# Performance work log

Hardware: AMD Instinct MI355X
Metric: run time of the kernel (lower is better)

Reference implementation:

```python
import jax, jax.numpy as jnp
import numpy as np

B, N, F, I = 4, 1024, 32, 8
DIM, DN, NF = 256, 64, 100
H, HD = 4, 64  # heads, head_dim (H*HD == DIM)
EPS = 1e-5


def setup_inputs() -> dict:
    key = jax.random.key(0)
    ks = jax.random.split(key, 24)
    def p(k, shape, s=0.05):
        return jax.random.normal(k, shape, jnp.float32) * s
    return {
        "x": jax.random.normal(ks[0], (B, N, F, I), jnp.float32),
        "idx": jax.random.randint(ks[1], (F,), 0, NF),
        "ctx": jax.random.normal(ks[2], (B, 1, DN), jnp.float32),
        "Wp": p(ks[3], (NF, DIM * I)),          # in_projection table
        "Bp": p(ks[4], (NF, DIM)),               # feature_bias table
        "q_emb": p(ks[5], (1, DIM)),             # queries table
        "cln_kv_W": p(ks[6], (DN, 2 * DIM)), "cln_kv_b": jnp.zeros((2 * DIM,), jnp.float32),
        "cln_q_W": p(ks[7], (DN, 2 * DIM)),  "cln_q_b": jnp.zeros((2 * DIM,), jnp.float32),
        "cln_h_W": p(ks[8], (DN, 2 * DIM)),  "cln_h_b": jnp.zeros((2 * DIM,), jnp.float32),
        "Wq": p(ks[9], (DIM, DIM)), "Wk": p(ks[10], (DIM, DIM)),
        "Wv": p(ks[11], (DIM, DIM)), "Wo": p(ks[12], (DIM, DIM)),
        "W1": p(ks[13], (DIM, 4 * DIM)), "b1": jnp.zeros((4 * DIM,), jnp.float32),
        "W2": p(ks[14], (4 * DIM, DIM)), "b2": jnp.zeros((DIM,), jnp.float32),
    }


def _ln(x):
    m = x.mean(-1, keepdims=True)
    v = ((x - m) ** 2).mean(-1, keepdims=True)
    return (x - m) * jax.lax.rsqrt(v + EPS)


def _cln(x, c, W, b):
    # adaptive layernorm: ln(x) * (1 + scale(ctx)) + shift(ctx)
    h = _ln(x)
    s, sh = jnp.split(c @ W + b, 2, axis=-1)
    return h * (1.0 + s) + sh


def reference(x, idx, ctx, Wp, Bp, q_emb, cln_kv_W, cln_kv_b, cln_q_W, cln_q_b,
              cln_h_W, cln_h_b, Wq, Wk, Wv, Wo, W1, b1, W2, b2):
    b_, n_, f_, i_ = x.shape
    # gather per-feature projection weights and biases
    w = Wp[idx].reshape(f_, DIM, i_)                 # [f, d, i]
    bias = Bp[idx][None]                              # [1, f, d] (broadcasts b,n)
    kv = jnp.einsum('bnfi,fdi->bnfd', x, w)           # [b, n, f, d]
    c = ctx[:, :, None, :]                            # [b, 1, 1, dn]
    kv = _cln(kv, c, cln_kv_W, cln_kv_b) + bias
    q = jnp.broadcast_to(q_emb[None, None], (b_, n_, 1, DIM))
    # cross-attention (pre-norm, conditional)
    qn = _cln(q, c, cln_q_W, cln_q_b)
    qh = (qn @ Wq).reshape(b_, n_, 1, H, HD)
    kh = (kv @ Wk).reshape(b_, n_, f_, H, HD)
    vh = (kv @ Wv).reshape(b_, n_, f_, H, HD)
    att = jnp.einsum('bnqhe,bnfhe->bnhqf', qh, kh) / np.sqrt(HD).astype(np.float32)
    att = jax.nn.softmax(att, axis=-1)
    o = jnp.einsum('bnhqf,bnfhe->bnqhe', att, vh).reshape(b_, n_, 1, DIM) @ Wo
    h = q + o
    # MLP (pre-norm, conditional)
    hn = _cln(h, c, cln_h_W, cln_h_b)
    h = h + (jax.nn.gelu(hn @ W1 + b1) @ W2 + b2)
    return h[:, :, 0, :]                              # squeeze query dim -> [b, n, d]
```

## Files before the change

### kernel.cpp

```cpp
#include <hip/hip_runtime.h>
#include <cmath>

#define EPSV 1e-5f
using f4 = float4;

typedef __attribute__((ext_vector_type(8))) short bfrag;
typedef __attribute__((ext_vector_type(4))) float ffrag;

#define WS_SKV   0
#define WS_SHKV  1024
#define WS_SH    2048
#define WS_SHH   3072
#define WS_A     4096
#define WS_R     8192
#define WS_HT    4202496
#define WS_L     5251072
#define WS_G     6299648
#define WS_GB    WS_G
#define WS_HNB   (WS_G + 2097152)
#define WS_W1T   (WS_G + 2621440)
#define WS_W2T   (WS_G + 2752512)
#define WS_MT    (WS_G + 2883584)

#define FMA8(acc, s, wa, wb) \
  acc[0]=fmaf((s),(wa).x,acc[0]); acc[1]=fmaf((s),(wa).y,acc[1]); \
  acc[2]=fmaf((s),(wa).z,acc[2]); acc[3]=fmaf((s),(wa).w,acc[3]); \
  acc[4]=fmaf((s),(wb).x,acc[4]); acc[5]=fmaf((s),(wb).y,acc[5]); \
  acc[6]=fmaf((s),(wb).z,acc[6]); acc[7]=fmaf((s),(wb).w,acc[7]);

#define DOT8(res, v, wa, wb) \
  res = fmaf((v)[0],(wa).x,res); res = fmaf((v)[1],(wa).y,res); \
  res = fmaf((v)[2],(wa).z,res); res = fmaf((v)[3],(wa).w,res); \
  res = fmaf((v)[4],(wb).x,res); res = fmaf((v)[5],(wb).y,res); \
  res = fmaf((v)[6],(wb).z,res); res = fmaf((v)[7],(wb).w,res);

__device__ __forceinline__ float bfly32(float v){
  v += __shfl_xor(v, 1);  v += __shfl_xor(v, 2);  v += __shfl_xor(v, 4);
  v += __shfl_xor(v, 8);  v += __shfl_xor(v, 16);
  return v;
}

template<int CTRL>
__device__ __forceinline__ float dpp_add(float v){
  int x = __builtin_bit_cast(int, v);
  int y = __builtin_amdgcn_update_dpp(0, x, CTRL, 0xf, 0xf, true);
  return v + __builtin_bit_cast(float, y);
}
__device__ __forceinline__ float red32(float v){
  v = dpp_add<0xB1>(v);
  v = dpp_add<0x4E>(v);
  v = dpp_add<0x124>(v);
  v = dpp_add<0x128>(v);
  v += __shfl_xor(v, 16);
  return v;
}

__device__ __forceinline__ float gelu_fast(float x){
  float z2 = 1.5957691216057308f*(x + 0.044715f*x*x*x);
  return x / (1.0f + __expf(-z2));
}

__device__ __forceinline__ unsigned short f2bf(float x){
  union { float f; unsigned u; } v; v.f = x;
  unsigned r = v.u + 0x7fffu + ((v.u >> 16) & 1u);
  return (unsigned short)(r >> 16);
}
__device__ __forceinline__ float bfu(unsigned short u){
  union { unsigned u; float f; } v; v.u = ((unsigned)u) << 16; return v.f;
}
__device__ __forceinline__ ushort4 comb4(ushort4 a, ushort4 b, float inv){
  ushort4 r;
  r.x = f2bf((bfu(a.x)+bfu(b.x))*inv);
  r.y = f2bf((bfu(a.y)+bfu(b.y))*inv);
  r.z = f2bf((bfu(a.z)+bfu(b.z))*inv);
  r.w = f2bf((bfu(a.w)+bfu(b.w))*inv);
  return r;
}

__global__ __launch_bounds__(256) void kwm_conv(
  const float* __restrict__ W1, const float* __restrict__ W2,
  const float* __restrict__ Wv, const float* __restrict__ Wo,
  float* __restrict__ ws)
{
  const int tid = threadIdx.x;
  int blk = blockIdx.x;
  if (blk < 128){
    __shared__ unsigned short lt[64][68];
    const float* src; unsigned short* dst; int K, N, K0, N0;
    if (blk < 64){
      src = W1; dst = (unsigned short*)(ws + WS_W1T);
      K = 256; N = 1024; K0 = (blk >> 4)*64; N0 = (blk & 15)*64;
    } else {
      blk -= 64;
      src = W2; dst = (unsigned short*)(ws + WS_W2T);
      K = 1024; N = 256; K0 = (blk >> 2)*64; N0 = (blk & 3)*64;
    }
    #pragma unroll
    for (int i=0;i<4;++i){
      int r = i*16 + (tid>>4);
      int c = (tid&15)*4;
      f4 v = *(const f4*)(src + (size_t)(K0+r)*N + N0 + c);
      lt[r][c]   = f2bf(v.x); lt[r][c+1] = f2bf(v.y);
      lt[r][c+2] = f2bf(v.z); lt[r][c+3] = f2bf(v.w);
    }
    __syncthreads();
    #pragma unroll
    for (int i=0;i<4;++i){
      int n  = i*16 + (tid>>4);
      int kc = (tid&15)*4;
      ushort4 u;
      u.x = lt[kc][n]; u.y = lt[kc+1][n]; u.z = lt[kc+2][n]; u.w = lt[kc+3][n];
      *(ushort4*)(dst + (size_t)(N0+n)*K + K0 + kc) = u;
    }
  } else {
    blk -= 128;
    __shared__ float wvs[4*64];
    __shared__ float wos[64*256];
    const int h   = blk >> 6;
    const int dg4 = blk & 63;
    {
      int d = tid >> 6, e = tid & 63;
      wvs[d*64+e] = Wv[(size_t)(dg4*4 + d)*256 + h*64 + e];
    }
    {
      int e = tid >> 2, c = (tid & 3)*64;
      const float* src = Wo + (size_t)(h*64 + e)*256 + c;
      #pragma unroll
      for (int i=0;i<16;++i)
        *(f4*)&wos[e*256 + c + i*4] = *(const f4*)(src + i*4);
    }
    __syncthreads();
    float acc[4] = {};
    for (int e=0;e<64;++e){
      float wo = wos[e*256 + tid];
      acc[0] = fmaf(wvs[0*64+e], wo, acc[0]);
      acc[1] = fmaf(wvs[1*64+e], wo, acc[1]);
      acc[2] = fmaf(wvs[2*64+e], wo, acc[2]);
      acc[3] = fmaf(wvs[3*64+e], wo, acc[3]);
    }
    unsigned short* Mt = (unsigned short*)(ws + WS_MT);
    ushort4 u;
    u.x = f2bf(acc[0]); u.y = f2bf(acc[1]); u.z = f2bf(acc[2]); u.w = f2bf(acc[3]);
    *(ushort4*)(Mt + (size_t)tid*1024 + h*256 + dg4*4) = u;
  }
}

__global__ __launch_bounds__(256) void k0_all(
    const float* __restrict__ ctx, const float* __restrict__ q_emb,
    const float* __restrict__ Wkv, const float* __restrict__ bkv,
    const float* __restrict__ Wqc, const float* __restrict__ bqc,
    const float* __restrict__ Whc, const float* __restrict__ bhc,
    const float* __restrict__ Wq,  const float* __restrict__ Wk,
    float* __restrict__ ws)
{
  const int b = blockIdx.x >> 2, h = blockIdx.x & 3;
  const int tid = threadIdx.x;
  __shared__ float c[64], qn[256], ph[256], qh64[64], red[8];
  if (tid < 64) c[tid] = ctx[b*64 + tid];
  __syncthreads();

  float skv = bkv[tid],      shkv = bkv[256+tid];
  float sq  = bqc[tid],      shq  = bqc[256+tid];
  float sh  = bhc[tid],      shh  = bhc[256+tid];
  #pragma unroll 8
  for (int j=0;j<64;++j){
    float cj = c[j];
    skv  = fmaf(cj, Wkv[j*512 + tid],       skv);
    shkv = fmaf(cj, Wkv[j*512 + 256 + tid], shkv);
    sq   = fmaf(cj, Wqc[j*512 + tid],       sq);
    shq  = fmaf(cj, Wqc[j*512 + 256 + tid], shq);
    sh   = fmaf(cj, Whc[j*512 + tid],       sh);
    shh  = fmaf(cj, Whc[j*512 + 256 + tid], shh);
  }
  if (h == 0){
    ws[WS_SKV  + b*256 + tid] = skv;
    ws[WS_SHKV + b*256 + tid] = shkv;
    ws[WS_SH   + b*256 + tid] = sh;
    ws[WS_SHH  + b*256 + tid] = shh;
  }

  float qe = q_emb[tid];
  float s1r = qe, s2r = qe*qe;
  for (int mm=1;mm<64;mm<<=1){ s1r += __shfl_xor(s1r,mm); s2r += __shfl_xor(s2r,mm); }
  int wv = tid>>6, ln = tid&63;
  if (ln==0){ red[wv*2]=s1r; red[wv*2+1]=s2r; }
  __syncthreads();
  float S1 = red[0]+red[2]+red[4]+red[6];
  float S2 = red[1]+red[3]+red[5]+red[7];
  float mean = S1*(1.0f/256.0f);
  float var  = S2*(1.0f/256.0f) - mean*mean;
  float rs   = rsqrtf(var + EPSV);
  qn[tid] = (qe-mean)*rs*(1.0f+sq) + shq;
  __syncthreads();

  {
    const int t = tid & 63, ks = tid >> 6;
    float p = 0.f;
    const float* wq = Wq + (size_t)(ks*64)*256 + h*64 + t;
    #pragma unroll 8
    for (int d=0; d<64; ++d) p = fmaf(qn[ks*64+d], wq[d*256], p);
    ph[tid] = p;
  }
  __syncthreads();
  if (tid < 64) qh64[tid] = ph[tid] + ph[64+tid] + ph[128+tid] + ph[192+tid];
  __syncthreads();

  {
    float a = 0.f;
    const float* wkr = Wk + (size_t)tid*256 + h*64;
    #pragma unroll
    for (int e4=0; e4<16; ++e4){
      f4 wv4 = *(const f4*)(wkr + e4*4);
      a = fmaf(qh64[e4*4+0], wv4.x, a);
      a = fmaf(qh64[e4*4+1], wv4.y, a);
      a = fmaf(qh64[e4*4+2], wv4.z, a);
      a = fmaf(qh64[e4*4+3], wv4.w, a);
    }
    ws[WS_A + b*1024 + h*256 + tid] = 0.125f*a;
  }
}

__global__ __launch_bounds__(256,4) void k1f_attn(
  const float* __restrict__ x, const int* __restrict__ idx,
  const float* __restrict__ Wp, const float* __restrict__ Bp,
  float* __restrict__ ws)
{
  __shared__ float xs[2048];
  __shared__ float wls[4096];

  const int tid = threadIdx.x;
  const int p0  = (blockIdx.x >> 1) * 8;
  const int half= blockIdx.x & 1;
  const int f0  = half * 16;
  const int b   = p0 >> 10;
  const int t   = tid >> 5;
  const int dg  = tid & 31;
  const int dA  = 4*dg, dB = 128 + 4*dg;

  {
    const float* xg = x + (size_t)p0*256 + tid*8;
    f4 a  = *(const f4*)xg;
    f4 bq = *(const f4*)(xg + 4);
    *(f4*)&xs[tid*8]     = a;
    *(f4*)&xs[tid*8 + 4] = bq;
  }
  f4 Ar[4][2];
  #pragma unroll
  for (int h=0;h<4;++h){
    Ar[h][0] = *(const f4*)(ws + WS_A + b*1024 + h*256 + dA);
    Ar[h][1] = *(const f4*)(ws + WS_A + b*1024 + h*256 + dB);
  }

  f4 skA = *(const f4*)(ws + WS_SKV  + b*256 + dA);
  f4 skB = *(const f4*)(ws + WS_SKV  + b*256 + dB);
  f4 shA = *(const f4*)(ws + WS_SHKV + b*256 + dA);
  f4 shB = *(const f4*)(ws + WS_SHKV + b*256 + dB);
  float coef[8] = {1.f+skA.x,1.f+skA.y,1.f+skA.z,1.f+skA.w,
                   1.f+skB.x,1.f+skB.y,1.f+skB.z,1.f+skB.w};
  float shk[8]  = {shA.x,shA.y,shA.z,shA.w, shB.x,shB.y,shB.z,shB.w};

  int r0 = idx[f0], r1 = idx[f0+1];
  f4 u0 = *(const f4*)(Wp + (size_t)r0*2048 + tid*8);
  f4 u1 = *(const f4*)(Wp + (size_t)r0*2048 + tid*8 + 4);
  f4 u2 = *(const f4*)(Wp + (size_t)r1*2048 + tid*8);
  f4 u3 = *(const f4*)(Wp + (size_t)r1*2048 + tid*8 + 4);

  float l[4] = {0.f,0.f,0.f,0.f};
  float racc[4][8] = {};

  for (int fi = 0; fi < 8; ++fi){
    const int f = f0 + fi*2;
    __syncthreads();
    wls[0*256+tid]=u0.x; wls[1*256+tid]=u0.y; wls[2*256+tid]=u0.z; wls[3*256+tid]=u0.w;
    wls[4*256+tid]=u1.x; wls[5*256+tid]=u1.y; wls[6*256+tid]=u1.z; wls[7*256+tid]=u1.w;
    wls[2048+0*256+tid]=u2.x; wls[2048+1*256+tid]=u2.y;
    wls[2048+2*256+tid]=u2.z; wls[2048+3*256+tid]=u2.w;
    wls[2048+4*256+tid]=u3.x; wls[2048+5*256+tid]=u3.y;
    wls[2048+6*256+tid]=u3.z; wls[2048+7*256+tid]=u3.w;
    __syncthreads();

    f4 ba0 = *(const f4*)(Bp + (size_t)r0*256 + dA);
    f4 bb0 = *(const f4*)(Bp + (size_t)r0*256 + dB);
    f4 ba1 = *(const f4*)(Bp + (size_t)r1*256 + dA);
    f4 bb1 = *(const f4*)(Bp + (size_t)r1*256 + dB);

    const int fn = (fi < 7) ? f + 2 : f0;
    int rn0 = idx[fn], rn1 = idx[fn+1];
    u0 = *(const f4*)(Wp + (size_t)rn0*2048 + tid*8);
    u1 = *(const f4*)(Wp + (size_t)rn0*2048 + tid*8 + 4);
    u2 = *(const f4*)(Wp + (size_t)rn1*2048 + tid*8);
    u3 = *(const f4*)(Wp + (size_t)rn1*2048 + tid*8 + 4);

    #pragma unroll
    for (int sub=0; sub<2; ++sub){
      const float* wrow = wls + sub*2048;
      const int fc = f + sub;
      f4 ba = sub ? ba1 : ba0;
      f4 bb = sub ? bb1 : bb0;

      f4 xa = *(const f4*)&xs[t*256 + fc*8];
      f4 xb = *(const f4*)&xs[t*256 + fc*8 + 4];
      float xf[8] = {xa.x,xa.y,xa.z,xa.w, xb.x,xb.y,xb.z,xb.w};

      float val[8] = {};
      #pragma unroll
      for (int i=0;i<8;++i){
        f4 wa  = *(const f4*)&wrow[i*256 + dA];
        f4 wbv = *(const f4*)&wrow[i*256 + dB];
        FMA8(val, xf[i], wa, wbv);
      }

      float s=0.f, ss=0.f;
      #pragma unroll
      for (int jj=0;jj<8;++jj){ s += val[jj]; ss = fmaf(val[jj],val[jj],ss); }
      s = red32(s); ss = red32(ss);
      float mean = s*(1.f/256.f);
      float var  = ss*(1.f/256.f) - mean*mean;
      float rsg  = rsqrtf(var + EPSV);
      float mrs  = mean*rsg;

      float off[8] = {shk[0]+ba.x, shk[1]+ba.y, shk[2]+ba.z, shk[3]+ba.w,
                      shk[4]+bb.x, shk[5]+bb.y, shk[6]+bb.z, shk[7]+bb.w};
      float kvl[8];
      #pragma unroll
      for (int jj=0;jj<8;++jj)
        kvl[jj] = fmaf(fmaf(val[jj], rsg, -mrs), coef[jj], off[jj]);

      #pragma unroll
      for (int h=0;h<4;++h){
        float lg = 0.f;
        DOT8(lg, kvl, Ar[h][0], Ar[h][1]);
        lg = red32(lg);
        float pp = __expf(lg);
        l[h] += pp;
        #pragma unroll
        for (int jj=0;jj<8;++jj)
          racc[h][jj] = fmaf(pp, kvl[jj], racc[h][jj]);
      }
    }
    r0 = rn0; r1 = rn1;
  }

  unsigned short* Pr = (unsigned short*)(ws + WS_R);
  size_t base = (size_t)(half*4096 + p0 + t) * 1024;
  #pragma unroll
  for (int h=0;h<4;++h){
    ushort4 ua, ub;
    ua.x=f2bf(racc[h][0]); ua.y=f2bf(racc[h][1]); ua.z=f2bf(racc[h][2]); ua.w=f2bf(racc[h][3]);
    ub.x=f2bf(racc[h][4]); ub.y=f2bf(racc[h][5]); ub.z=f2bf(racc[h][6]); ub.w=f2bf(racc[h][7]);
    *(ushort4*)(Pr + base + h*256 + dA) = ua;
    *(ushort4*)(Pr + base + h*256 + dB) = ub;
  }
  if (dg == 0){
    float* Lp = ws + WS_L;
    #pragma unroll
    for (int h=0;h<4;++h) Lp[(size_t)(half*4096 + p0 + t)*4 + h] = l[h];
  }
}

__global__ __launch_bounds__(256) void k2g_mfma(float* __restrict__ ws)
{
  __shared__ unsigned short aT[2][32*40];
  __shared__ unsigned short bT[2][64*40];
  __shared__ float invs[128];
  const unsigned short* P0 = (const unsigned short*)(ws + WS_R);
  const unsigned short* P1 = P0 + 4194304;
  const unsigned short* mt = (const unsigned short*)(ws + WS_MT);
  const float* Lp = ws + WS_L;

  const int tid = threadIdx.x;
  const int M0 = (blockIdx.x >> 2) * 32;
  const int N0 = (blockIdx.x & 3) * 64;
  const int lane = tid & 63;
  const int wid = tid >> 6;
  const int wm = wid >> 1, wn = wid & 1;
  const int m16 = lane & 15, q = lane >> 4;

  const int sa_m = tid >> 3, sa_k = (tid & 7) * 4;
  const int sb_n = tid >> 2, sb_k = (tid & 3) * 8;

  if (tid < 128){
    int lt = tid >> 2, h = tid & 3;
    invs[tid] = 1.f / (Lp[(size_t)(M0 + lt)*4 + h] +
                       Lp[(size_t)(4096 + M0 + lt)*4 + h]);
  }

  ushort4 ua0 = *(const ushort4*)(P0 + (size_t)(M0 + sa_m)*1024 + sa_k);
  ushort4 ua1 = *(const ushort4*)(P1 + (size_t)(M0 + sa_m)*1024 + sa_k);
  f4 ub = *(const f4*)(mt + (size_t)(N0 + sb_n)*1024 + sb_k);
  __syncthreads();

  ffrag acc[2];
  acc[0] = (ffrag){0.f,0.f,0.f,0.f};
  acc[1] = (ffrag){0.f,0.f,0.f,0.f};

  for (int ks=0; ks<32; ++ks){
    const int buf = ks & 1;
    float inv = invs[sa_m*4 + (ks >> 3)];
    *(ushort4*)&aT[buf][sa_m*40 + sa_k] = comb4(ua0, ua1, inv);
    *(f4*)&bT[buf][sb_n*40 + sb_k]      = ub;
    __syncthreads();
    int kn = (ks < 31) ? ks+1 : 31;
    ua0 = *(const ushort4*)(P0 + (size_t)(M0 + sa_m)*1024 + kn*32 + sa_k);
    ua1 = *(const ushort4*)(P1 + (size_t)(M0 + sa_m)*1024 + kn*32 + sa_k);
    ub  = *(const f4*)(mt + (size_t)(N0 + sb_n)*1024 + kn*32 + sb_k);

    bfrag af, bf0, bf1;
    af  = *(const bfrag*)&aT[buf][(wm*16 + m16)*40 + q*8];
    bf0 = *(const bfrag*)&bT[buf][(wn*32 + m16)*40 + q*8];
    bf1 = *(const bfrag*)&bT[buf][(wn*32 + 16 + m16)*40 + q*8];
    acc[0] = __builtin_amdgcn_mfma_f32_16x16x32_bf16(bf0, af, acc[0], 0, 0, 0);
    acc[1] = __builtin_amdgcn_mfma_f32_16x16x32_bf16(bf1, af, acc[1], 0, 0, 0);
  }

  const int m = M0 + wm*16 + m16;
  #pragma unroll
  for (int j=0;j<2;++j){
    const int n4 = N0 + wn*32 + j*16 + q*4;
    *(f4*)(ws + WS_HT + (size_t)m*256 + n4) =
      make_float4(acc[j][0], acc[j][1], acc[j][2], acc[j][3]);
  }
}

__global__ __launch_bounds__(256) void ke_ln(
  const float* __restrict__ q_emb, float* __restrict__ ws)
{
  const int tid = threadIdx.x;
  const int p0 = blockIdx.x * 8;
  const int b  = p0 >> 10;
  const int tq = tid >> 5, jq = tid & 31;
  const int cA = 4*jq, cB = 128 + 4*jq;

  float* op = ws + WS_HT + (size_t)(p0+tq)*256;
  f4 oA = *(const f4*)(op + cA);
  f4 oB = *(const f4*)(op + cB);
  f4 qA = *(const f4*)(q_emb + cA);
  f4 qB = *(const f4*)(q_emb + cB);
  float ht[8] = {oA.x+qA.x, oA.y+qA.y, oA.z+qA.z, oA.w+qA.w,
                 oB.x+qB.x, oB.y+qB.y, oB.z+qB.z, oB.w+qB.w};
  float s=0.f, ss=0.f;
  #pragma unroll
  for (int jj=0;jj<8;++jj){ s += ht[jj]; ss = fmaf(ht[jj],ht[jj],ss); }
  s = bfly32(s); ss = bfly32(ss);
  float mean = s*(1.f/256.f);
  float var  = ss*(1.f/256.f) - mean*mean;
  float rsg  = rsqrtf(var + EPSV);
  f4 sH0 = *(const f4*)(ws + WS_SH  + b*256 + cA);
  f4 sH1 = *(const f4*)(ws + WS_SH  + b*256 + cB);
  f4 hH0 = *(const f4*)(ws + WS_SHH + b*256 + cA);
  f4 hH1 = *(const f4*)(ws + WS_SHH + b*256 + cB);
  float sHv[8]  = {sH0.x,sH0.y,sH0.z,sH0.w, sH1.x,sH1.y,sH1.z,sH1.w};
  float hHv[8]  = {hH0.x,hH0.y,hH0.z,hH0.w, hH1.x,hH1.y,hH1.z,hH1.w};
  float hnv[8];
  #pragma unroll
  for (int jj=0;jj<8;++jj)
    hnv[jj] = (ht[jj]-mean)*rsg*(1.f+sHv[jj]) + hHv[jj];

  *(f4*)(op+cA) = make_float4(ht[0],ht[1],ht[2],ht[3]);
  *(f4*)(op+cB) = make_float4(ht[4],ht[5],ht[6],ht[7]);
  unsigned short* hnb = (unsigned short*)(ws + WS_HNB);
  ushort4 uA, uB;
  uA.x=f2bf(hnv[0]); uA.y=f2bf(hnv[1]); uA.z=f2bf(hnv[2]); uA.w=f2bf(hnv[3]);
  uB.x=f2bf(hnv[4]); uB.y=f2bf(hnv[5]); uB.z=f2bf(hnv[6]); uB.w=f2bf(hnv[7]);
  *(ushort4*)(hnb + (size_t)(p0+tq)*256 + cA) = uA;
  *(ushort4*)(hnb + (size_t)(p0+tq)*256 + cB) = uB;
}

__global__ __launch_bounds__(256) void k3_mfma(
  const float* __restrict__ b1, float* __restrict__ ws)
{
  __shared__ unsigned short aT[2][64*40];
  __shared__ unsigned short bT[2][128*40];
  const unsigned short* hnb = (const unsigned short*)(ws + WS_HNB);
  const unsigned short* w1t = (const unsigned short*)(ws + WS_W1T);
  unsigned short* gb = (unsigned short*)(ws + WS_GB);

  const int tid = threadIdx.x;
  const int M0 = (blockIdx.x >> 3) * 64;
  const int N0 = (blockIdx.x & 7) * 128;
  const int lane = tid & 63;
  const int wid = tid >> 6;
  const int wm = wid >> 1, wn = wid & 1;
  const int m16 = lane & 15, q = lane >> 4;

  const int sa_m = tid >> 2, sa_k = (tid & 3) * 8;
  const int sb_n = tid >> 1, sb_k = (tid & 1) * 16;

  f4 ua, ub0, ub1;
  ua  = *(const f4*)(hnb + (size_t)(M0 + sa_m)*256 + sa_k);
  ub0 = *(const f4*)(w1t + (size_t)(N0 + sb_n)*256 + sb_k);
  ub1 = *(const f4*)(w1t + (size_t)(N0 + sb_n)*256 + sb_k + 8);

  ffrag acc[2][4];
  #pragma unroll
  for (int i=0;i<2;++i)
    #pragma unroll
    for (int j=0;j<4;++j) acc[i][j] = (ffrag){0.f,0.f,0.f,0.f};

  for (int ks=0; ks<8; ++ks){
    const int buf = ks & 1;
    *(f4*)&aT[buf][sa_m*40 + sa_k]     = ua;
    *(f4*)&bT[buf][sb_n*40 + sb_k]     = ub0;
    *(f4*)&bT[buf][sb_n*40 + sb_k + 8] = ub1;
    __syncthreads();
    int kn = (ks < 7) ? ks+1 : 7;
    ua  = *(const f4*)(hnb + (size_t)(M0 + sa_m)*256 + kn*32 + sa_k);
    ub0 = *(const f4*)(w1t + (size_t)(N0 + sb_n)*256 + kn*32 + sb_k);
    ub1 = *(const f4*)(w1t + (size_t)(N0 + sb_n)*256 + kn*32 + sb_k + 8);

    bfrag af[2], bf_[4];
    af[0] = *(const bfrag*)&aT[buf][(wm*32 + m16)*40 + q*8];
    af[1] = *(const bfrag*)&aT[buf][(wm*32 + 16 + m16)*40 + q*8];
    #pragma unroll
    for (int j=0;j<4;++j)
      bf_[j] = *(const bfrag*)&bT[buf][(wn*64 + j*16 + m16)*40 + q*8];
    #pragma unroll
    for (int i=0;i<2;++i)
      #pragma unroll
      for (int j=0;j<4;++j)
        acc[i][j] = __builtin_amdgcn_mfma_f32_16x16x32_bf16(bf_[j], af[i], acc[i][j], 0, 0, 0);
  }

  #pragma unroll
  for (int i=0;i<2;++i){
    const int m = M0 + wm*32 + i*16 + m16;
    #pragma unroll
    for (int j=0;j<4;++j){
      const int n4 = N0 + wn*64 + j*16 + q*4;
      f4 bv = *(const f4*)(b1 + n4);
      ushort4 u;
      u.x = f2bf(gelu_fast(acc[i][j][0] + bv.x));
      u.y = f2bf(gelu_fast(acc[i][j][1] + bv.y));
      u.z = f2bf(gelu_fast(acc[i][j][2] + bv.z));
      u.w = f2bf(gelu_fast(acc[i][j][3] + bv.w));
      *(ushort4*)(gb + (size_t)m*1024 + n4) = u;
    }
  }
}

__global__ __launch_bounds__(256) void k4_mfma(
  const float* __restrict__ b2, const float* __restrict__ ws_c,
  float* __restrict__ ws, float* __restrict__ out)
{
  __shared__ unsigned short aT[2][32*40];
  __shared__ unsigned short bT[2][64*40];
  const unsigned short* gb  = (const unsigned short*)(ws_c + WS_GB);
  const unsigned short* w2t = (const unsigned short*)(ws_c + WS_W2T);

  const int tid = threadIdx.x;
  const int M0 = (blockIdx.x >> 2) * 32;
  const int N0 = (blockIdx.x & 3) * 64;
  const int lane = tid & 63;
  const int wid = tid >> 6;
  const int wm = wid >> 1, wn = wid & 1;
  const int m16 = lane & 15, q = lane >> 4;

  const int sa_m = tid >> 3, sa_k = (tid & 7) * 4;
  const int sb_n = tid >> 2, sb_k = (tid & 3) * 8;

  ushort4 ua;
  f4 ub;
  ua = *(const ushort4*)(gb  + (size_t)(M0 + sa_m)*1024 + sa_k);
  ub = *(const f4*)(w2t + (size_t)(N0 + sb_n)*1024 + sb_k);

  ffrag acc[2];
  acc[0] = (ffrag){0.f,0.f,0.f,0.f};
  acc[1] = (ffrag){0.f,0.f,0.f,0.f};

  for (int ks=0; ks<32; ++ks){
    const int buf = ks & 1;
    *(ushort4*)&aT[buf][sa_m*40 + sa_k] = ua;
    *(f4*)&bT[buf][sb_n*40 + sb_k]      = ub;
    __syncthreads();
    int kn = (ks < 31) ? ks+1 : 31;
    ua = *(const ushort4*)(gb  + (size_t)(M0 + sa_m)*1024 + kn*32 + sa_k);
    ub = *(const f4*)(w2t + (size_t)(N0 + sb_n)*1024 + kn*32 + sb_k);

    bfrag af, bf0, bf1;
    af  = *(const bfrag*)&aT[buf][(wm*16 + m16)*40 + q*8];
    bf0 = *(const bfrag*)&bT[buf][(wn*32 + m16)*40 + q*8];
    bf1 = *(const bfrag*)&bT[buf][(wn*32 + 16 + m16)*40 + q*8];
    acc[0] = __builtin_amdgcn_mfma_f32_16x16x32_bf16(bf0, af, acc[0], 0, 0, 0);
    acc[1] = __builtin_amdgcn_mfma_f32_16x16x32_bf16(bf1, af, acc[1], 0, 0, 0);
  }

  const int m = M0 + wm*16 + m16;
  #pragma unroll
  for (int j=0;j<2;++j){
    const int n4 = N0 + wn*32 + j*16 + q*4;
    f4 bv = *(const f4*)(b2 + n4);
    f4 hv = *(const f4*)(ws + WS_HT + (size_t)m*256 + n4);
    *(f4*)(out + (size_t)m*256 + n4) =
      make_float4(acc[j][0]+bv.x+hv.x, acc[j][1]+bv.y+hv.y,
                  acc[j][2]+bv.z+hv.z, acc[j][3]+bv.w+hv.w);
  }
}

extern "C" void kernel_launch(void* const* d_in, const int* in_sizes, int n_in,
                              void* d_out, int out_size, void* d_ws, size_t ws_size,
                              hipStream_t stream)
{
  const float* x    = (const float*)d_in[0];
  const int*   idx  = (const int*)  d_in[1];
  const float* ctx  = (const float*)d_in[2];
  const float* Wp   = (const float*)d_in[3];
  const float* Bp   = (const float*)d_in[4];
  const float* qemb = (const float*)d_in[5];
  const float* Wkv  = (const float*)d_in[6];
  const float* bkv  = (const float*)d_in[7];
  const float* Wqc  = (const float*)d_in[8];
  const float* bqc  = (const float*)d_in[9];
  const float* Whc  = (const float*)d_in[10];
  const float* bhc  = (const float*)d_in[11];
  const float* Wq   = (const float*)d_in[12];
  const float* Wk   = (const float*)d_in[13];
  const float* Wv   = (const float*)d_in[14];
  const float* Wo   = (const float*)d_in[15];
  const float* W1   = (const float*)d_in[16];
  const float* b1   = (const float*)d_in[17];
  const float* W2   = (const float*)d_in[18];
  const float* b2   = (const float*)d_in[19];
  float* ws  = (float*)d_ws;
  float* out = (float*)d_out;

  hipLaunchKernelGGL(kwm_conv, dim3(384),  dim3(256), 0, stream, W1, W2, Wv, Wo, ws);
  hipLaunchKernelGGL(k0_all,   dim3(16),   dim3(256), 0, stream,
                     ctx, qemb, Wkv, bkv, Wqc, bqc, Whc, bhc, Wq, Wk, ws);
  hipLaunchKernelGGL(k1f_attn, dim3(1024), dim3(256), 0, stream, x, idx, Wp, Bp, ws);
  hipLaunchKernelGGL(k2g_mfma, dim3(512),  dim3(256), 0, stream, ws);
  hipLaunchKernelGGL(ke_ln,    dim3(512),  dim3(256), 0, stream, qemb, ws);
  hipLaunchKernelGGL(k3_mfma,  dim3(512),  dim3(256), 0, stream, b1, ws);
  hipLaunchKernelGGL(k4_mfma,  dim3(512),  dim3(256), 0, stream, b2, ws, ws, out);
}
```

Baseline: 193.8 us.

## Merge prep kernels and process two token rows per thread in attention kernel

Folds the context/query precompute kernel into the weight-conversion kernel as extra blocks sharing a union of shared memory, removing one launch. The attention kernel now handles 16 tokens per block (two per thread) so each weight row read from shared memory is reused for two tokens, halving the grid. This raises register pressure (launch bounds lowered to 2 blocks per SM) and cuts parallelism to 512 blocks, which may hurt latency hiding.

Measured after the change: 187.0 us. 3.5% less time.

```diff
diff --git a/kernel.cpp b/kernel.cpp
--- a/kernel.cpp
+++ b/kernel.cpp
@@ -77,15 +77,25 @@
   return r;
 }
 
-__global__ __launch_bounds__(256) void kwm_conv(
+__global__ __launch_bounds__(256) void kprep(
   const float* __restrict__ W1, const float* __restrict__ W2,
   const float* __restrict__ Wv, const float* __restrict__ Wo,
+  const float* __restrict__ ctx, const float* __restrict__ q_emb,
+  const float* __restrict__ Wkv, const float* __restrict__ bkv,
+  const float* __restrict__ Wqc, const float* __restrict__ bqc,
+  const float* __restrict__ Whc, const float* __restrict__ bhc,
+  const float* __restrict__ Wq,  const float* __restrict__ Wk,
   float* __restrict__ ws)
 {
   const int tid = threadIdx.x;
   int blk = blockIdx.x;
+  __shared__ union {
+    unsigned short lt[64][68];
+    struct { float wvs[4*64]; float wos[64*256]; } m;
+    struct { float c[64], qn[256], ph[256], qh64[64], red[8]; } z;
+  } sm;
+
   if (blk < 128){
-    __shared__ unsigned short lt[64][68];
     const float* src; unsigned short* dst; int K, N, K0, N0;
     if (blk < 64){
       src = W1; dst = (unsigned short*)(ws + WS_W1T);
@@ -100,8 +110,8 @@
       int r = i*16 + (tid>>4);
       int c = (tid&15)*4;
       f4 v = *(const f4*)(src + (size_t)(K0+r)*N + N0 + c);
-      lt[r][c]   = f2bf(v.x); lt[r][c+1] = f2bf(v.y);
-      lt[r][c+2] = f2bf(v.z); lt[r][c+3] = f2bf(v.w);
+      sm.lt[r][c]   = f2bf(v.x); sm.lt[r][c+1] = f2bf(v.y);
+      sm.lt[r][c+2] = f2bf(v.z); sm.lt[r][c+3] = f2bf(v.w);
     }
     __syncthreads();
     #pragma unroll
@@ -109,127 +119,115 @@
       int n  = i*16 + (tid>>4);
       int kc = (tid&15)*4;
       ushort4 u;
-      u.x = lt[kc][n]; u.y = lt[kc+1][n]; u.z = lt[kc+2][n]; u.w = lt[kc+3][n];
+      u.x = sm.lt[kc][n]; u.y = sm.lt[kc+1][n]; u.z = sm.lt[kc+2][n]; u.w = sm.lt[kc+3][n];
       *(ushort4*)(dst + (size_t)(N0+n)*K + K0 + kc) = u;
     }
-  } else {
+  } else if (blk < 384){
     blk -= 128;
-    __shared__ float wvs[4*64];
-    __shared__ float wos[64*256];
     const int h   = blk >> 6;
     const int dg4 = blk & 63;
     {
       int d = tid >> 6, e = tid & 63;
-      wvs[d*64+e] = Wv[(size_t)(dg4*4 + d)*256 + h*64 + e];
+      sm.m.wvs[d*64+e] = Wv[(size_t)(dg4*4 + d)*256 + h*64 + e];
     }
     {
       int e = tid >> 2, c = (tid & 3)*64;
       const float* src = Wo + (size_t)(h*64 + e)*256 + c;
       #pragma unroll
       for (int i=0;i<16;++i)
-        *(f4*)&wos[e*256 + c + i*4] = *(const f4*)(src + i*4);
+        *(f4*)&sm.m.wos[e*256 + c + i*4] = *(const f4*)(src + i*4);
     }
     __syncthreads();
     float acc[4] = {};
     for (int e=0;e<64;++e){
-      float wo = wos[e*256 + tid];
-      acc[0] = fmaf(wvs[0*64+e], wo, acc[0]);
-      acc[1] = fmaf(wvs[1*64+e], wo, acc[1]);
-      acc[2] = fmaf(wvs[2*64+e], wo, acc[2]);
-      acc[3] = fmaf(wvs[3*64+e], wo, acc[3]);
+      float wo = sm.m.wos[e*256 + tid];
+      acc[0] = fmaf(sm.m.wvs[0*64+e], wo, acc[0]);
+      acc[1] = fmaf(sm.m.wvs[1*64+e], wo, acc[1]);
+      acc[2] = fmaf(sm.m.wvs[2*64+e], wo, acc[2]);
+      acc[3] = fmaf(sm.m.wvs[3*64+e], wo, acc[3]);
     }
     unsigned short* Mt = (unsigned short*)(ws + WS_MT);
     ushort4 u;
     u.x = f2bf(acc[0]); u.y = f2bf(acc[1]); u.z = f2bf(acc[2]); u.w = f2bf(acc[3]);
     *(ushort4*)(Mt + (size_t)tid*1024 + h*256 + dg4*4) = u;
-  }
-}
-
-__global__ __launch_bounds__(256) void k0_all(
-    const float* __restrict__ ctx, const float* __restrict__ q_emb,
-    const float* __restrict__ Wkv, const float* __restrict__ bkv,
-    const float* __restrict__ Wqc, const float* __restrict__ bqc,
-    const float* __restrict__ Whc, const float* __restrict__ bhc,
-    const float* __restrict__ Wq,  const float* __restrict__ Wk,
-    float* __restrict__ ws)
-{
-  const int b = blockIdx.x >> 2, h = blockIdx.x & 3;
-  const int tid = threadIdx.x;
-  __shared__ float c[64], qn[256], ph[256], qh64[64], red[8];
-  if (tid < 64) c[tid] = ctx[b*64 + tid];
-  __syncthreads();
-
-  float skv = bkv[tid],      shkv = bkv[256+tid];
-  float sq  = bqc[tid],      shq  = bqc[256+tid];
-  float sh  = bhc[tid],      shh  = bhc[256+tid];
-  #pragma unroll 8
-  for (int j=0;j<64;++j){
-    float cj = c[j];
-    skv  = fmaf(cj, Wkv[j*512 + tid],       skv);
-    shkv = fmaf(cj, Wkv[j*512 + 256 + tid], shkv);
-    sq   = fmaf(cj, Wqc[j*512 + tid],       sq);
-    shq  = fmaf(cj, Wqc[j*512 + 256 + tid], shq);
-    sh   = fmaf(cj, Whc[j*512 + tid],       sh);
-    shh  = fmaf(cj, Whc[j*512 + 256 + tid], shh);
-  }
-  if (h == 0){
-    ws[WS_SKV  + b*256 + tid] = skv;
-    ws[WS_SHKV + b*256 + tid] = shkv;
-    ws[WS_SH   + b*256 + tid] = sh;
-    ws[WS_SHH  + b*256 + tid] = shh;
-  }
-
-  float qe = q_emb[tid];
-  float s1r = qe, s2r = qe*qe;
-  for (int mm=1;mm<64;mm<<=1){ s1r += __shfl_xor(s1r,mm); s2r += __shfl_xor(s2r,mm); }
-  int wv = tid>>6, ln = tid&63;
-  if (ln==0){ red[wv*2]=s1r; red[wv*2+1]=s2r; }
-  __syncthreads();
-  float S1 = red[0]+red[2]+red[4]+red[6];
-  float S2 = red[1]+red[3]+red[5]+red[7];
-  float mean = S1*(1.0f/256.0f);
-  float var  = S2*(1.0f/256.0f) - mean*mean;
-  float rs   = rsqrtf(var + EPSV);
-  qn[tid] = (qe-mean)*rs*(1.0f+sq) + shq;
-  __syncthreads();
-
-  {
-    const int t = tid & 63, ks = tid >> 6;
-    float p = 0.f;
-    const float* wq = Wq + (size_t)(ks*64)*256 + h*64 + t;
+  } else {
+    blk -= 384;
+    const int b = blk >> 2, h = blk & 3;
+    if (tid < 64) sm.z.c[tid] = ctx[b*64 + tid];
+    __syncthreads();
+
+    float skv = bkv[tid],      shkv = bkv[256+tid];
+    float sq  = bqc[tid],      shq  = bqc[256+tid];
+    float sh  = bhc[tid],      shh  = bhc[256+tid];
     #pragma unroll 8
-    for (int d=0; d<64; ++d) p = fmaf(qn[ks*64+d], wq[d*256], p);
-    ph[tid] = p;
-  }
-  __syncthreads();
-  if (tid < 64) qh64[tid] = ph[tid] + ph[64+tid] + ph[128+tid] + ph[192+tid];
-  __syncthreads();
-
-  {
-    float a = 0.f;
-    const float* wkr = Wk + (size_t)tid*256 + h*64;
-    #pragma unroll
-    for (int e4=0; e4<16; ++e4){
-      f4 wv4 = *(const f4*)(wkr + e4*4);
-      a = fmaf(qh64[e4*4+0], wv4.x, a);
-      a = fmaf(qh64[e4*4+1], wv4.y, a);
-      a = fmaf(qh64[e4*4+2], wv4.z, a);
-      a = fmaf(qh64[e4*4+3], wv4.w, a);
-    }
-    ws[WS_A + b*1024 + h*256 + tid] = 0.125f*a;
-  }
-}
-
-__global__ __launch_bounds__(256,4) void k1f_attn(
+    for (int j=0;j<64;++j){
+      float cj = sm.z.c[j];
+      skv  = fmaf(cj, Wkv[j*512 + tid],       skv);
+      shkv = fmaf(cj, Wkv[j*512 + 256 + tid], shkv);
+      sq   = fmaf(cj, Wqc[j*512 + tid],       sq);
+      shq  = fmaf(cj, Wqc[j*512 + 256 + tid], shq);
+      sh   = fmaf(cj, Whc[j*512 + tid],       sh);
+      shh  = fmaf(cj, Whc[j*512 + 256 + tid], shh);
+    }
+    if (h == 0){
+      ws[WS_SKV  + b*256 + tid] = skv;
+      ws[WS_SHKV + b*256 + tid] = shkv;
+      ws[WS_SH   + b*256 + tid] = sh;
+      ws[WS_SHH  + b*256 + tid] = shh;
+    }
+
+    float qe = q_emb[tid];
+    float s1r = qe, s2r = qe*qe;
+    for (int mm=1;mm<64;mm<<=1){ s1r += __shfl_xor(s1r,mm); s2r += __shfl_xor(s2r,mm); }
+    int wv = tid>>6, ln = tid&63;
+    if (ln==0){ sm.z.red[wv*2]=s1r; sm.z.red[wv*2+1]=s2r; }
+    __syncthreads();
+    float S1 = sm.z.red[0]+sm.z.red[2]+sm.z.red[4]+sm.z.red[6];
+    float S2 = sm.z.red[1]+sm.z.red[3]+sm.z.red[5]+sm.z.red[7];
+    float mean = S1*(1.0f/256.0f);
+    float var  = S2*(1.0f/256.0f) - mean*mean;
+    float rs   = rsqrtf(var + EPSV);
+    sm.z.qn[tid] = (qe-mean)*rs*(1.0f+sq) + shq;
+    __syncthreads();
+
+    {
+      const int t = tid & 63, ks = tid >> 6;
+      float p = 0.f;
+      const float* wq = Wq + (size_t)(ks*64)*256 + h*64 + t;
+      #pragma unroll 8
+      for (int d=0; d<64; ++d) p = fmaf(sm.z.qn[ks*64+d], wq[d*256], p);
+      sm.z.ph[tid] = p;
+    }
+    __syncthreads();
+    if (tid < 64) sm.z.qh64[tid] = sm.z.ph[tid] + sm.z.ph[64+tid] + sm.z.ph[128+tid] + sm.z.ph[192+tid];
+    __syncthreads();
+
+    {
+      float a = 0.f;
+      const float* wkr = Wk + (size_t)tid*256 + h*64;
+      #pragma unroll
+      for (int e4=0; e4<16; ++e4){
+        f4 wv4 = *(const f4*)(wkr + e4*4);
+        a = fmaf(sm.z.qh64[e4*4+0], wv4.x, a);
+        a = fmaf(sm.z.qh64[e4*4+1], wv4.y, a);
+        a = fmaf(sm.z.qh64[e4*4+2], wv4.z, a);
+        a = fmaf(sm.z.qh64[e4*4+3], wv4.w, a);
+      }
+      ws[WS_A + b*1024 + h*256 + tid] = 0.125f*a;
+    }
+  }
+}
+
+__global__ __launch_bounds__(256,2) void k1f_attn(
   const float* __restrict__ x, const int* __restrict__ idx,
   const float* __restrict__ Wp, const float* __restrict__ Bp,
   float* __restrict__ ws)
 {
-  __shared__ float xs[2048];
+  __shared__ float xs[4096];
   __shared__ float wls[4096];
 
   const int tid = threadIdx.x;
-  const int p0  = (blockIdx.x >> 1) * 8;
+  const int p0  = (blockIdx.x >> 1) * 16;
   const int half= blockIdx.x & 1;
   const int f0  = half * 16;
   const int b   = p0 >> 10;
@@ -243,6 +241,10 @@
     f4 bq = *(const f4*)(xg + 4);
     *(f4*)&xs[tid*8]     = a;
     *(f4*)&xs[tid*8 + 4] = bq;
+    f4 a2  = *(const f4*)(xg + 2048);
+    f4 bq2 = *(const f4*)(xg + 2048 + 4);
+    *(f4*)&xs[2048 + tid*8]     = a2;
+    *(f4*)&xs[2048 + tid*8 + 4] = bq2;
   }
   f4 Ar[4][2];
   #pragma unroll
@@ -265,8 +267,8 @@
   f4 u2 = *(const f4*)(Wp + (size_t)r1*2048 + tid*8);
   f4 u3 = *(const f4*)(Wp + (size_t)r1*2048 + tid*8 + 4);
 
-  float l[4] = {0.f,0.f,0.f,0.f};
-  float racc[4][8] = {};
+  float l[2][4] = {};
+  float racc[2][4][8] = {};
 
   for (int fi = 0; fi < 8; ++fi){
     const int f = f0 + fi*2;
@@ -298,63 +300,84 @@
       f4 ba = sub ? ba1 : ba0;
       f4 bb = sub ? bb1 : bb0;
 
-      f4 xa = *(const f4*)&xs[t*256 + fc*8];
-      f4 xb = *(const f4*)&xs[t*256 + fc*8 + 4];
-      float xf[8] = {xa.x,xa.y,xa.z,xa.w, xb.x,xb.y,xb.z,xb.w};
-
-      float val[8] = {};
+      float xf0[8], xf1[8];
+      {
+        f4 xa = *(const f4*)&xs[t*256 + fc*8];
+        f4 xb = *(const f4*)&xs[t*256 + fc*8 + 4];
+        xf0[0]=xa.x; xf0[1]=xa.y; xf0[2]=xa.z; xf0[3]=xa.w;
+        xf0[4]=xb.x; xf0[5]=xb.y; xf0[6]=xb.z; xf0[7]=xb.w;
+        f4 xc = *(const f4*)&xs[(t+8)*256 + fc*8];
+        f4 xd = *(const f4*)&xs[(t+8)*256 + fc*8 + 4];
+        xf1[0]=xc.x; xf1[1]=xc.y; xf1[2]=xc.z; xf1[3]=xc.w;
+        xf1[4]=xd.x; xf1[5]=xd.y; xf1[6]=xd.z; xf1[7]=xd.w;
+      }
+
+      float val[2][8] = {};
       #pragma unroll
       for (int i=0;i<8;++i){
         f4 wa  = *(const f4*)&wrow[i*256 + dA];
         f4 wbv = *(const f4*)&wrow[i*256 + dB];
-        FMA8(val, xf[i], wa, wbv);
+        FMA8(val[0], xf0[i], wa, wbv);
+        FMA8(val[1], xf1[i], wa, wbv);
       }
-
-      float s=0.f, ss=0.f;
-      #pragma unroll
-      for (int jj=0;jj<8;++jj){ s += val[jj]; ss = fmaf(val[jj],val[jj],ss); }
-      s = red32(s); ss = red32(ss);
-      float mean = s*(1.f/256.f);
-      float var  = ss*(1.f/256.f) - mean*mean;
-      float rsg  = rsqrtf(var + EPSV);
-      float mrs  = mean*rsg;
 
       float off[8] = {shk[0]+ba.x, shk[1]+ba.y, shk[2]+ba.z, shk[3]+ba.w,
                       shk[4]+bb.x, shk[5]+bb.y, shk[6]+bb.z, shk[7]+bb.w};
-      float kvl[8];
+
       #pragma unroll
-      for (int jj=0;jj<8;++jj)
-        kvl[jj] = fmaf(fmaf(val[jj], rsg, -mrs), coef[jj], off[jj]);
-
-      #pragma unroll
-      for (int h=0;h<4;++h){
-        float lg = 0.f;
-        DOT8(lg, kvl, Ar[h][0], Ar[h][1]);
-        lg = red32(lg);
-        float pp = __expf(lg);
-        l[h] += pp;
+      for (int tt=0; tt<2; ++tt){
+        float s=0.f, ss=0.f;
+        #pragma unroll
+        for (int jj=0;jj<8;++jj){ s += val[tt][jj]; ss = fmaf(val[tt][jj],val[tt][jj],ss); }
+        s = red32(s); ss = red32(ss);
+        float mean = s*(1.f/256.f);
+        float var  = ss*(1.f/256.f) - mean*mean;
+        float rsg  = rsqrtf(var + EPSV);
+        float mrs  = mean*rsg;
+
+        float kvl[8];
         #pragma unroll
         for (int jj=0;jj<8;++jj)
-          racc[h][jj] = fmaf(pp, kvl[jj], racc[h][jj]);
+          kvl[jj] = fmaf(fmaf(val[tt][jj], rsg, -mrs), coef[jj], off[jj]);
+
+        #pragma unroll
+        for (int h=0;h<4;++h){
+          float lg = 0.f;
+          DOT8(lg, kvl, Ar[h][0], Ar[h][1]);
+          lg = red32(lg);
+          float pp = __expf(lg);
+          l[tt][h] += pp;
+          #pragma unroll
+          for (int jj=0;jj<8;++jj)
+            racc[tt][h][jj] = fmaf(pp, kvl[jj], racc[tt][h][jj]);
+        }
       }
     }
     r0 = rn0; r1 = rn1;
   }
 
   unsigned short* Pr = (unsigned short*)(ws + WS_R);
-  size_t base = (size_t)(half*4096 + p0 + t) * 1024;
-  #pragma unroll
-  for (int h=0;h<4;++h){
-    ushort4 ua, ub;
-    ua.x=f2bf(racc[h][0]); ua.y=f2bf(racc[h][1]); ua.z=f2bf(racc[h][2]); ua.w=f2bf(racc[h][3]);
-    ub.x=f2bf(racc[h][4]); ub.y=f2bf(racc[h][5]); ub.z=f2bf(racc[h][6]); ub.w=f2bf(racc[h][7]);
-    *(ushort4*)(Pr + base + h*256 + dA) = ua;
-    *(ushort4*)(Pr + base + h*256 + dB) = ub;
+  #pragma unroll
+  for (int tt=0; tt<2; ++tt){
+    size_t base = (size_t)(half*4096 + p0 + t + tt*8) * 1024;
+    #pragma unroll
+    for (int h=0;h<4;++h){
+      ushort4 ua, ub;
+      ua.x=f2bf(racc[tt][h][0]); ua.y=f2bf(racc[tt][h][1]);
+      ua.z=f2bf(racc[tt][h][2]); ua.w=f2bf(racc[tt][h][3]);
+      ub.x=f2bf(racc[tt][h][4]); ub.y=f2bf(racc[tt][h][5]);
+      ub.z=f2bf(racc[tt][h][6]); ub.w=f2bf(racc[tt][h][7]);
+      *(ushort4*)(Pr + base + h*256 + dA) = ua;
+      *(ushort4*)(Pr + base + h*256 + dB) = ub;
+    }
   }
   if (dg == 0){
     float* Lp = ws + WS_L;
     #pragma unroll
-    for (int h=0;h<4;++h) Lp[(size_t)(half*4096 + p0 + t)*4 + h] = l[h];
+    for (int tt=0; tt<2; ++tt)
+      #pragma unroll
+      for (int h=0;h<4;++h)
+        Lp[(size_t)(half*4096 + p0 + t + tt*8)*4 + h] = l[tt][h];
   }
 }
 
@@ -623,10 +646,9 @@
   float* ws  = (float*)d_ws;
   float* out = (float*)d_out;
 
-  hipLaunchKernelGGL(kwm_conv, dim3(384),  dim3(256), 0, stream, W1, W2, Wv, Wo, ws);
-  hipLaunchKernelGGL(k0_all,   dim3(16),   dim3(256), 0, stream,
-                     ctx, qemb, Wkv, bkv, Wqc, bqc, Whc, bhc, Wq, Wk, ws);
-  hipLaunchKernelGGL(k1f_attn, dim3(1024), dim3(256), 0, stream, x, idx, Wp, Bp, ws);
+  hipLaunchKernelGGL(kprep,    dim3(400),  dim3(256), 0, stream,
+                     W1, W2, Wv, Wo, ctx, qemb, Wkv, bkv, Wqc, bqc, Whc, bhc, Wq, Wk, ws);
+  hipLaunchKernelGGL(k1f_attn, dim3(512),  dim3(256), 0, stream, x, idx, Wp, Bp, ws);
   hipLaunchKernelGGL(k2g_mfma, dim3(512),  dim3(256), 0, stream, ws);
   hipLaunchKernelGGL(ke_ln,    dim3(512),  dim3(256), 0, stream, qemb, ws);
   hipLaunchKernelGGL(k3_mfma,  dim3(512),  dim3(256), 0, stream, b1, ws);
```
